# Performance work log

Hardware: AMD Instinct MI355X
Metric: run time of the kernel (lower is better)

## Reference

```python
import jax, jax.numpy as jnp
import numpy as np

H = 256
NUM_CONVS = 4
NUM_GRAPHS = 1024
N_PER_GRAPH = 32
ORDER = 3
NUM_TYPES = 22  # len(utils.BOND_TYPES)
NUM_NOISE_LEVEL = 50
ANNEAL_POWER = 2.0


def _build_graph():
    # Chain molecules extended to order-3 neighbors (mimics extend_graph on a path graph):
    # for |i-j| in [1,ORDER]: edge_order=|i-j|, edge_type = bond type if order 1 else NUM_TYPES+order-1.
    n = N_PER_GRAPH
    i, j = np.meshgrid(np.arange(n), np.arange(n), indexing='ij')
    dist = np.abs(i - j)
    mask = (dist >= 1) & (dist <= ORDER)
    src_l, dst_l, eo = i[mask], j[mask], dist[mask]
    offs = np.arange(NUM_GRAPHS)[:, None] * n
    src = (src_l[None, :] + offs).reshape(-1)
    dst = (dst_l[None, :] + offs).reshape(-1)
    edge_order = np.tile(eo, NUM_GRAPHS)
    rng = np.random.default_rng(0)
    bond_t = rng.integers(1, 5, size=edge_order.shape)
    edge_type = np.where(edge_order == 1, bond_t, NUM_TYPES + edge_order - 1)
    node2graph = np.repeat(np.arange(NUM_GRAPHS), n)
    return src, dst, edge_type, node2graph


def setup_inputs() -> dict:
    key = jax.random.key(0)
    ks = jax.random.split(key, 24)
    src, dst, edge_type, node2graph = _build_graph()
    N, E = node2graph.shape[0], src.shape[0]
    w = lambda k, s: (jax.random.normal(k, s, jnp.float32) * 0.05)
    sigmas = jnp.asarray(np.exp(np.linspace(np.log(10.0), np.log(0.01), NUM_NOISE_LEVEL)), dtype=jnp.float32)
    return {
        'atom_type': jnp.asarray(np.random.default_rng(1).integers(0, 100, N), jnp.int32),
        'edge_index': jnp.asarray(np.stack([src, dst]), jnp.int32),
        'edge_type': jnp.asarray(edge_type, jnp.int32),
        'node2graph': jnp.asarray(node2graph, jnp.int32),
        'noise_level': jax.random.randint(ks[0], (NUM_GRAPHS,), 0, NUM_NOISE_LEVEL, jnp.int32),
        'pos': jax.random.normal(ks[1], (N, 3), jnp.float32) * 3.0,
        'd_noise': jax.random.normal(ks[2], (E, 1), jnp.float32),
        'sigmas': sigmas,
        'node_emb': w(ks[3], (100, H)), 'edge_emb': w(ks[4], (100, H)),
        'in_W1': w(ks[5], (1, H)), 'in_b1': w(ks[6], (H,)),
        'in_W2': w(ks[7], (H, H)), 'in_b2': w(ks[8], (H,)),
        'gin_W1': w(ks[9], (NUM_CONVS, H, H)), 'gin_b1': w(ks[10], (NUM_CONVS, H)),
        'gin_W2': w(ks[11], (NUM_CONVS, H, H)), 'gin_b2': w(ks[12], (NUM_CONVS, H)),
        'out_W1': w(ks[13], (2 * H, H)), 'out_b1': w(ks[14], (H,)),
        'out_W2': w(ks[15], (H, H // 2)), 'out_b2': w(ks[16], (H // 2,)),
        'out_W3': w(ks[17], (H // 2, 1)), 'out_b3': w(ks[18], (1,)),
    }


def reference(atom_type, edge_index, edge_type, node2graph, noise_level,
              pos, d_noise, sigmas, node_emb, edge_emb,
              in_W1, in_b1, in_W2, in_b2,
              gin_W1, gin_b1, gin_W2, gin_b2,
              out_W1, out_b1, out_W2, out_b2, out_W3, out_b3):
    N = pos.shape[0]
    G = noise_level.shape[0]
    row, col = edge_index[0], edge_index[1]
    edge2graph = node2graph[row]                                  # [E]
    d = jnp.linalg.norm(pos[row] - pos[col], axis=-1, keepdims=True)  # [E,1]
    used_sigmas = sigmas[noise_level][edge2graph][:, None]        # [E,1]
    perturbed_d = d + d_noise * used_sigmas
    target = -(perturbed_d - d) / used_sigmas ** 2
    # embeddings + input MLP (Linear-relu-Linear)
    node_attr = node_emb[atom_type]                               # [N,H]
    d_emb = jax.nn.relu(perturbed_d @ in_W1 + in_b1) @ in_W2 + in_b2
    edge_attr = d_emb * edge_emb[edge_type]                       # [E,H]
    # GIN with GINE convs: agg = sum_j relu(x_j + e_ij); out = MLP(x + agg); relu between convs; residual
    x = node_attr
    n_convs = gin_W1.shape[0]
    for k in range(n_convs):
        msg = jax.nn.relu(x[row] + edge_attr)                     # [E,H]
        agg = jax.ops.segment_sum(msg, col, num_segments=N)       # [N,H]
        h = jax.nn.relu((x + agg) @ gin_W1[k] + gin_b1[k]) @ gin_W2[k] + gin_b2[k]
        if k < n_convs - 1:
            h = jax.nn.relu(h)
        x = h + x  # short_cut
    # edge score head
    feat = jnp.concatenate([x[row] * x[col], edge_attr], axis=-1)  # [E,2H]
    s = jax.nn.relu(feat @ out_W1 + out_b1)
    s = jax.nn.relu(s @ out_W2 + out_b2)
    s = s @ out_W3 + out_b3                                       # [E,1]
    scores = (s / used_sigmas).reshape(-1)
    t = target.reshape(-1)
    loss_e = 0.5 * (scores - t) ** 2 * used_sigmas.reshape(-1) ** ANNEAL_POWER
    return jax.ops.segment_sum(loss_e, edge2graph, num_segments=G)  # [G]
```

## Files before the change

### kernel.cpp

```cpp
#include <hip/hip_runtime.h>
#include <math.h>

typedef unsigned int u32;
typedef __attribute__((ext_vector_type(8))) short bf16x8;
typedef __attribute__((ext_vector_type(4))) float f32x4;

#define MFMA16(a,b,c) __builtin_amdgcn_mfma_f32_16x16x32_bf16(a,b,c,0,0,0)

__device__ inline u32 bf16r(float x){
  u32 u = __float_as_uint(x);
  return (u + 0x7fffu + ((u >> 16) & 1u)) >> 16;
}
__device__ inline u32 pack2(float a, float b){ return bf16r(a) | (bf16r(b) << 16); }
__device__ inline uint4 pack8(const float* f){
  uint4 v; v.x = pack2(f[0],f[1]); v.y = pack2(f[2],f[3]);
  v.z = pack2(f[4],f[5]); v.w = pack2(f[6],f[7]); return v;
}

__device__ __forceinline__ void gload_lds16(const void* g, void* l){
  __builtin_amdgcn_global_load_lds((const __attribute__((address_space(1))) unsigned int*)g,
                                   (__attribute__((address_space(3))) unsigned int*)l,
                                   16, 0, 0);
}

__device__ __forceinline__ int frag_off(int f, int quad){
  return (f>>1)*64 + (f&1)*32 + ((quad ^ ((f>>1)&3))*8);
}

__global__ void k_cvtAll(const float* __restrict__ inW2, const float* __restrict__ gW1,
                         const float* __restrict__ gW2, const float* __restrict__ oW1,
                         const float* __restrict__ oW2,
                         short* __restrict__ w2t, short* __restrict__ gw1t,
                         short* __restrict__ gw2t, short* __restrict__ ow1t,
                         short* __restrict__ ow2t){
  int gidx = blockIdx.x*256 + threadIdx.x;
  const float* src; short* dst; int t, K8, Nf;
  if (gidx < 8192)      { src = inW2; dst = w2t; t = gidx; K8 = 32; Nf = 256; }
  else if (gidx < 40960){ int r = gidx-8192;  int c = r>>13; t = r&8191;
                          src = gW1 + (size_t)c*65536; dst = gw1t + (size_t)c*65536; K8 = 32; Nf = 256; }
  else if (gidx < 73728){ int r = gidx-40960; int c = r>>13; t = r&8191;
                          src = gW2 + (size_t)c*65536; dst = gw2t + (size_t)c*65536; K8 = 32; Nf = 256; }
  else if (gidx < 90112){ t = gidx-73728; src = oW1; dst = ow1t; K8 = 64; Nf = 256; }
  else if (gidx < 94208){ t = gidx-90112; src = oW2; dst = ow2t; K8 = 32; Nf = 128; }
  else return;
  int f = t / K8, c = t - f*K8;
  float v[8];
  #pragma unroll
  for (int j=0;j<8;j++) v[j] = src[(size_t)(c*8+j)*Nf + f];
  ((uint4*)dst)[t] = pack8(v);
}

__global__ void k_pre(const int* __restrict__ ei, const int* __restrict__ n2g,
                      const int* __restrict__ nl, const float* __restrict__ sigmas,
                      const float* __restrict__ pos, const float* __restrict__ dn, int E,
                      float* __restrict__ pd, int* __restrict__ cnt, int* __restrict__ inlist){
  int e = blockIdx.x*256 + threadIdx.x;
  if (e >= E) return;
  int r = ei[e], c = ei[E+e];
  float sg = sigmas[nl[n2g[r]]];
  float dx = pos[3*r]-pos[3*c], dy = pos[3*r+1]-pos[3*c+1], dz = pos[3*r+2]-pos[3*c+2];
  float d = sqrtf(dx*dx + dy*dy + dz*dz);
  pd[e] = d + dn[e]*sg;
  int slot = atomicAdd(&cnt[c], 1);
  if (slot < 8) inlist[c*8 + slot] = e;
}

__global__ void k_ninit(const int* __restrict__ at, const float* __restrict__ nemb,
                        float* __restrict__ x, int N){
  int idx = blockIdx.x*256 + threadIdx.x;
  int i = idx >> 6, c = idx & 63;
  if (i >= N) return;
  ((float4*)x)[(size_t)i*64 + c] = ((const float4*)nemb)[(size_t)at[i]*64 + c];
}

__global__ __launch_bounds__(256) void k_attr(
    const float* __restrict__ pd, const float* __restrict__ W1, const float* __restrict__ b1,
    const short* __restrict__ W2t, const float* __restrict__ b2,
    const int* __restrict__ etype, const float* __restrict__ eemb,
    short* __restrict__ attr, int E)
{
  int tid = threadIdx.x;
  int base = blockIdx.x*64;
  int wv = tid>>6, lane = tid&63, quad = lane>>4, l15 = lane&15;
  float pdv[4];
  #pragma unroll
  for (int nt=0;nt<4;nt++) pdv[nt] = pd[base + nt*16 + l15];
  f32x4 acc[4][4];
  #pragma unroll
  for (int mt=0;mt<4;mt++) for (int nt=0;nt<4;nt++) acc[mt][nt] = (f32x4)0.f;
  #pragma unroll
  for (int s=0; s<8; s++){
    int k0 = s*32 + quad*8;
    float4 w1a = *(const float4*)(W1 + k0), w1b = *(const float4*)(W1 + k0 + 4);
    float4 b1a = *(const float4*)(b1 + k0), b1b = *(const float4*)(b1 + k0 + 4);
    bf16x8 a[4], b[4];
    #pragma unroll
    for (int mt=0;mt<4;mt++){
      int f = (wv*4+mt)*16 + l15;
      a[mt] = *(const bf16x8*)(W2t + (size_t)f*256 + k0);
    }
    #pragma unroll
    for (int nt=0;nt<4;nt++){
      float p = pdv[nt];
      float f[8] = {fmaxf(p*w1a.x+b1a.x,0.f), fmaxf(p*w1a.y+b1a.y,0.f),
                    fmaxf(p*w1a.z+b1a.z,0.f), fmaxf(p*w1a.w+b1a.w,0.f),
                    fmaxf(p*w1b.x+b1b.x,0.f), fmaxf(p*w1b.y+b1b.y,0.f),
                    fmaxf(p*w1b.z+b1b.z,0.f), fmaxf(p*w1b.w+b1b.w,0.f)};
      uint4 u = pack8(f);
      b[nt] = *(bf16x8*)&u;
    }
    #pragma unroll
    for (int mt=0;mt<4;mt++)
      #pragma unroll
      for (int nt=0;nt<4;nt++)
        acc[mt][nt] = MFMA16(a[mt], b[nt], acc[mt][nt]);
  }
  #pragma unroll
  for (int nt=0;nt<4;nt++){
    int e = base + nt*16 + l15;
    int et = etype[e];
    #pragma unroll
    for (int mt=0;mt<4;mt++){
      int f0 = (wv*4+mt)*16 + quad*4;
      float4 bb = *(const float4*)(b2 + f0);
      float4 em = *(const float4*)(eemb + (size_t)et*256 + f0);
      float v0 = (acc[mt][nt][0]+bb.x)*em.x, v1 = (acc[mt][nt][1]+bb.y)*em.y;
      float v2 = (acc[mt][nt][2]+bb.z)*em.z, v3 = (acc[mt][nt][3]+bb.w)*em.w;
      uint2 v; v.x = pack2(v0,v1); v.y = pack2(v2,v3);
      *(uint2*)(attr + (size_t)e*256 + f0) = v;
    }
  }
}

__global__ __launch_bounds__(256,3) void k_mlp(
    const float* __restrict__ x_in, const short* __restrict__ attrS,
    const int* __restrict__ ei, const int* __restrict__ cnt, const int* __restrict__ inlist,
    const short* __restrict__ W1t, const float* __restrict__ b1,
    const short* __restrict__ W2t, const float* __restrict__ b2,
    float* __restrict__ x_out, int N, int do_relu)
{
  __shared__ uint4 AlsV[64*32];
  short* Als = (short*)AlsV;
  short* T1  = Als;
  int tid = threadIdx.x;
  int base = blockIdx.x*64;
  for (int h=0; h<2; h++){
    int el = h*32 + (tid>>3), ch = tid&7;
    int j = base + el;
    float f[32];
    const float4* xj = (const float4*)x_in + (size_t)j*64 + ch*8;
    #pragma unroll
    for (int i=0;i<8;i++){ float4 v = xj[i]; f[i*4]=v.x; f[i*4+1]=v.y; f[i*4+2]=v.z; f[i*4+3]=v.w; }
    int deg = min(cnt[j], 8);
    for (int sIt=0; sIt<deg; sIt++){
      int e = inlist[j*8 + sIt];
      int r = ei[e];
      const float4* xr = (const float4*)x_in + (size_t)r*64 + ch*8;
      const short* ar = attrS + (size_t)e*256 + ch*32;
      #pragma unroll
      for (int i=0;i<8;i++){
        float4 xv = xr[i]; uint2 a = *(const uint2*)(ar + i*4);
        f[i*4]   += fmaxf(xv.x + __uint_as_float(a.x<<16), 0.f);
        f[i*4+1] += fmaxf(xv.y + __uint_as_float(a.x&0xffff0000u), 0.f);
        f[i*4+2] += fmaxf(xv.z + __uint_as_float(a.y<<16), 0.f);
        f[i*4+3] += fmaxf(xv.w + __uint_as_float(a.y&0xffff0000u), 0.f);
      }
    }
    #pragma unroll
    for (int qq=0;qq<4;qq++)
      *(uint4*)(Als + el*256 + (((ch*4+qq) ^ (el&7))*8)) = pack8(f + qq*8);
  }
  __syncthreads();
  int wv = tid>>6, lane = tid&63, quad = lane>>4, l15 = lane&15;
  f32x4 acc[4][4];
  #pragma unroll
  for (int mt=0;mt<4;mt++) for (int nt=0;nt<4;nt++) acc[mt][nt] = (f32x4)0.f;
  #pragma unroll
  for (int s=0; s<8; s++){
    bf16x8 a[4], b[4];
    #pragma unroll
    for (int mt=0;mt<4;mt++)
      a[mt] = *(const bf16x8*)(W1t + (size_t)((wv*4+mt)*16 + l15)*256 + s*32 + quad*8);
    #pragma unroll
    for (int nt=0;nt<4;nt++){
      int n = nt*16 + l15; int cc = s*4 + quad;
      b[nt] = *(const bf16x8*)(Als + n*256 + ((cc ^ (n&7))*8));
    }
    #pragma unroll
    for (int mt=0;mt<4;mt++)
      #pragma unroll
      for (int nt=0;nt<4;nt++)
        acc[mt][nt] = MFMA16(a[mt], b[nt], acc[mt][nt]);
  }
  __syncthreads();
  #pragma unroll
  for (int mt=0;mt<4;mt++){
    int f0 = (wv*4+mt)*16 + quad*4;
    float4 bb = *(const float4*)(b1 + f0);
    int c = f0 >> 3, off = (quad&1)*4;
    #pragma unroll
    for (int nt=0;nt<4;nt++){
      int n = nt*16 + l15;
      float v0 = fmaxf(acc[mt][nt][0]+bb.x,0.f), v1 = fmaxf(acc[mt][nt][1]+bb.y,0.f);
      float v2 = fmaxf(acc[mt][nt][2]+bb.z,0.f), v3 = fmaxf(acc[mt][nt][3]+bb.w,0.f);
      uint2 v; v.x = pack2(v0,v1); v.y = pack2(v2,v3);
      *(uint2*)(T1 + n*256 + ((c ^ (n&7))*8) + off) = v;
    }
  }
  __syncthreads();
  f32x4 acc2[4][4];
  #pragma unroll
  for (int mt=0;mt<4;mt++) for (int nt=0;nt<4;nt++) acc2[mt][nt] = (f32x4)0.f;
  #pragma unroll
  for (int s=0; s<8; s++){
    bf16x8 a[4], b[4];
    #pragma unroll
    for (int mt=0;mt<4;mt++)
      a[mt] = *(const bf16x8*)(W2t + (size_t)((wv*4+mt)*16 + l15)*256 + s*32 + quad*8);
    #pragma unroll
    for (int nt=0;nt<4;nt++){
      int n = nt*16 + l15; int cc = s*4 + quad;
      b[nt] = *(const bf16x8*)(T1 + n*256 + ((cc ^ (n&7))*8));
    }
    #pragma unroll
    for (int mt=0;mt<4;mt++)
      #pragma unroll
      for (int nt=0;nt<4;nt++)
        acc2[mt][nt] = MFMA16(a[mt], b[nt], acc2[mt][nt]);
  }
  #pragma unroll
  for (int mt=0;mt<4;mt++){
    int f0 = (wv*4+mt)*16 + quad*4;
    float4 bb = *(const float4*)(b2 + f0);
    #pragma unroll
    for (int nt=0;nt<4;nt++){
      int r = base + nt*16 + l15;
      const float* pin = x_in + (size_t)r*256 + f0;
      float* pout = x_out + (size_t)r*256 + f0;
      float4 xv = *(const float4*)pin;
      float h0 = acc2[mt][nt][0]+bb.x, h1 = acc2[mt][nt][1]+bb.y;
      float h2 = acc2[mt][nt][2]+bb.z, h3 = acc2[mt][nt][3]+bb.w;
      if (do_relu){ h0=fmaxf(h0,0.f); h1=fmaxf(h1,0.f); h2=fmaxf(h2,0.f); h3=fmaxf(h3,0.f); }
      xv.x += h0; xv.y += h1; xv.z += h2; xv.w += h3;
      *(float4*)pout = xv;
    }
  }
}

__global__ __launch_bounds__(256,2) void k_head(
    const float* __restrict__ x, const short* __restrict__ attrS,
    const int* __restrict__ ei,
    const short* __restrict__ W1t, const float* __restrict__ ob1,
    const short* __restrict__ W2t, const float* __restrict__ ob2,
    const float* __restrict__ W3, const float* __restrict__ ob3,
    const float* __restrict__ dnoise, const int* __restrict__ n2g,
    float* __restrict__ out, int E, int G)
{
  __shared__ uint4 BlsV[16*256];
  __shared__ float Sedge[64];
  __shared__ float part[4];
  short* Bls = (short*)BlsV;
  short* T   = (short*)BlsV;
  int tid = threadIdx.x;
  int base = blockIdx.x*64;
  int wv = tid>>6, lane = tid&63, quad = lane>>4, l15 = lane&15;
  if (tid < 64) Sedge[tid] = 0.f;
  if (tid < 4) part[tid] = 0.f;
  {
    int g = wv*64 + lane;
    int p = g>>3, hi = (g>>2)&1, cs = g&3;
    int n = p*2 + hi, cc = cs ^ (p&3);
    const short* srcb = attrS + (size_t)(base+n)*256 + cc*8;
    #pragma unroll
    for (int s=8; s<16; s++)
      gload_lds16(srcb + (s-8)*32, (char*)Bls + (size_t)s*4096 + wv*1024);
  }
  {
    int g = tid;
    int p = g>>3, hi = (g>>2)&1, cs = g&3;
    int n = p*2 + hi, cc = cs ^ (p&3);
    int rr = ei[base+n], rc = ei[E+base+n];
    const float* xr = x + (size_t)rr*256 + cc*8;
    const float* xc = x + (size_t)rc*256 + cc*8;
    #pragma unroll
    for (int s=0; s<8; s++){
      float4 a0 = *(const float4*)(xr + s*32), a1 = *(const float4*)(xr + s*32 + 4);
      float4 b0 = *(const float4*)(xc + s*32), b1 = *(const float4*)(xc + s*32 + 4);
      float f[8] = {a0.x*b0.x, a0.y*b0.y, a0.z*b0.z, a0.w*b0.w,
                    a1.x*b1.x, a1.y*b1.y, a1.z*b1.z, a1.w*b1.w};
      *(uint4*)(Bls + (size_t)s*2048 + g*8) = pack8(f);
    }
  }
  __syncthreads();
  f32x4 acc[4][4];
  #pragma unroll
  for (int mt=0;mt<4;mt++) for (int nt=0;nt<4;nt++) acc[mt][nt] = (f32x4)0.f;
  #pragma unroll
  for (int s=0; s<16; s++){
    bf16x8 a[4], b[4];
    #pragma unroll
    for (int mt=0;mt<4;mt++)
      a[mt] = *(const bf16x8*)(W1t + (size_t)((wv*4+mt)*16 + l15)*512 + s*32 + quad*8);
    #pragma unroll
    for (int nt=0;nt<4;nt++)
      b[nt] = *(const bf16x8*)(Bls + (size_t)s*2048 + frag_off(nt*16 + l15, quad));
    #pragma unroll
    for (int mt=0;mt<4;mt++)
      #pragma unroll
      for (int nt=0;nt<4;nt++)
        acc[mt][nt] = MFMA16(a[mt], b[nt], acc[mt][nt]);
  }
  __syncthreads();
  #pragma unroll
  for (int mt=0;mt<4;mt++){
    int f0 = (wv*4+mt)*16 + quad*4;
    float4 bb = *(const float4*)(ob1 + f0);
    int c = f0 >> 3, off = (quad&1)*4;
    #pragma unroll
    for (int nt=0;nt<4;nt++){
      int n = nt*16 + l15;
      float v0 = fmaxf(acc[mt][nt][0]+bb.x,0.f), v1 = fmaxf(acc[mt][nt][1]+bb.y,0.f);
      float v2 = fmaxf(acc[mt][nt][2]+bb.z,0.f), v3 = fmaxf(acc[mt][nt][3]+bb.w,0.f);
      uint2 v; v.x = pack2(v0,v1); v.y = pack2(v2,v3);
      *(uint2*)(T + n*256 + ((c ^ (n&7))*8) + off) = v;
    }
  }
  __syncthreads();
  f32x4 acc2[2][4];
  #pragma unroll
  for (int mt=0;mt<2;mt++) for (int nt=0;nt<4;nt++) acc2[mt][nt] = (f32x4)0.f;
  #pragma unroll
  for (int s=0; s<8; s++){
    bf16x8 a[2], b[4];
    #pragma unroll
    for (int mt=0;mt<2;mt++)
      a[mt] = *(const bf16x8*)(W2t + (size_t)((wv*2+mt)*16 + l15)*256 + s*32 + quad*8);
    #pragma unroll
    for (int nt=0;nt<4;nt++){
      int n = nt*16 + l15; int cc = s*4 + quad;
      b[nt] = *(const bf16x8*)(T + n*256 + ((cc ^ (n&7))*8));
    }
    #pragma unroll
    for (int mt=0;mt<2;mt++)
      #pragma unroll
      for (int nt=0;nt<4;nt++)
        acc2[mt][nt] = MFMA16(a[mt], b[nt], acc2[mt][nt]);
  }
  float4 b2v[2], w3v[2];
  #pragma unroll
  for (int mt=0;mt<2;mt++){
    int f0 = (wv*2+mt)*16 + quad*4;
    b2v[mt] = *(const float4*)(ob2 + f0);
    w3v[mt] = *(const float4*)(W3 + f0);
  }
  #pragma unroll
  for (int nt=0;nt<4;nt++){
    float p = 0.f;
    #pragma unroll
    for (int mt=0;mt<2;mt++){
      p += fmaxf(acc2[mt][nt][0]+b2v[mt].x,0.f)*w3v[mt].x;
      p += fmaxf(acc2[mt][nt][1]+b2v[mt].y,0.f)*w3v[mt].y;
      p += fmaxf(acc2[mt][nt][2]+b2v[mt].z,0.f)*w3v[mt].z;
      p += fmaxf(acc2[mt][nt][3]+b2v[mt].w,0.f)*w3v[mt].w;
    }
    p += __shfl_xor(p, 16);
    p += __shfl_xor(p, 32);
    if (lane < 16) atomicAdd(&Sedge[nt*16 + l15], p);
  }
  __syncthreads();
  int gbase = n2g[ei[base]];
  if (tid < 64){
    int e = base + tid;
    float sv = Sedge[tid] + ob3[0] + dnoise[e];
    float l = 0.5f*sv*sv;
    int g = n2g[ei[e]] - gbase;
    atomicAdd(&part[g & 3], l);
  }
  __syncthreads();
  if (tid < 2 && (gbase + tid) < G)
    atomicAdd(&out[gbase + tid], part[tid]);
}

static inline size_t alignup(size_t v){ return (v + 255) & ~(size_t)255; }

extern "C" void kernel_launch(void* const* d_in, const int* in_sizes, int n_in,
                              void* d_out, int out_size, void* d_ws, size_t ws_size,
                              hipStream_t stream) {
  const int*   at    = (const int*)  d_in[0];
  const int*   ei    = (const int*)  d_in[1];
  const int*   etype = (const int*)  d_in[2];
  const int*   n2g   = (const int*)  d_in[3];
  const int*   nl    = (const int*)  d_in[4];
  const float* pos   = (const float*)d_in[5];
  const float* dnoi  = (const float*)d_in[6];
  const float* sig   = (const float*)d_in[7];
  const float* nemb  = (const float*)d_in[8];
  const float* eemb  = (const float*)d_in[9];
  const float* inW1  = (const float*)d_in[10];
  const float* inb1  = (const float*)d_in[11];
  const float* inW2  = (const float*)d_in[12];
  const float* inb2  = (const float*)d_in[13];
  const float* gW1   = (const float*)d_in[14];
  const float* gb1   = (const float*)d_in[15];
  const float* gW2   = (const float*)d_in[16];
  const float* gb2   = (const float*)d_in[17];
  const float* oW1   = (const float*)d_in[18];
  const float* ob1   = (const float*)d_in[19];
  const float* oW2   = (const float*)d_in[20];
  const float* ob2   = (const float*)d_in[21];
  const float* oW3   = (const float*)d_in[22];
  const float* ob3   = (const float*)d_in[23];
  float* out = (float*)d_out;

  const int N = in_sizes[0];
  const int E = in_sizes[2];
  const int G = in_sizes[4];
  const int H = 256;

  char* w = (char*)d_ws;
  size_t off = 0;
  size_t o_attr  = off; off = alignup(off + (size_t)E*H*2);
  size_t o_xA    = off; off = alignup(off + (size_t)N*H*4);
  size_t o_xB    = off; off = alignup(off + (size_t)N*H*4);
  size_t o_pd    = off; off = alignup(off + (size_t)E*4);
  size_t o_cnt   = off; off = alignup(off + (size_t)N*4);
  size_t o_inl   = off; off = alignup(off + (size_t)N*8*4);
  size_t o_w2t   = off; off = alignup(off + (size_t)H*H*2);
  size_t o_gw1t  = off; off = alignup(off + (size_t)4*H*H*2);
  size_t o_gw2t  = off; off = alignup(off + (size_t)4*H*H*2);
  size_t o_ow1t  = off; off = alignup(off + (size_t)H*2*H*2);
  size_t o_ow2t  = off; off = alignup(off + (size_t)(H/2)*H*2);
  (void)ws_size; (void)n_in; (void)out_size;

  short* attrS = (short*)(w + o_attr);
  float* xA    = (float*)(w + o_xA);
  float* xB    = (float*)(w + o_xB);
  float* pd    = (float*)(w + o_pd);
  int*   cnt   = (int*)  (w + o_cnt);
  int*   inl   = (int*)  (w + o_inl);
  short* w2t   = (short*)(w + o_w2t);
  short* gw1t  = (short*)(w + o_gw1t);
  short* gw2t  = (short*)(w + o_gw2t);
  short* ow1t  = (short*)(w + o_ow1t);
  short* ow2t  = (short*)(w + o_ow2t);

  hipMemsetAsync(cnt, 0, (size_t)N*4, stream);
  hipMemsetAsync(out, 0, (size_t)G*4, stream);

  k_cvtAll<<<368, 256, 0, stream>>>(inW2, gW1, gW2, oW1, oW2,
                                    w2t, gw1t, gw2t, ow1t, ow2t);

  k_pre<<<(E+255)/256, 256, 0, stream>>>(ei, n2g, nl, sig, pos, dnoi, E, pd, cnt, inl);
  k_ninit<<<(N*64+255)/256, 256, 0, stream>>>(at, nemb, xA, N);
  k_attr<<<E/64, 256, 0, stream>>>(pd, inW1, inb1, w2t, inb2, etype, eemb, attrS, E);

  float* bufs[2] = {xA, xB};
  for (int c=0; c<4; c++){
    float* xin  = bufs[c & 1];
    float* xout = bufs[(c & 1) ^ 1];
    k_mlp<<<N/64, 256, 0, stream>>>(xin, attrS, ei, cnt, inl,
        gw1t + (size_t)c*H*H, gb1 + (size_t)c*H,
        gw2t + (size_t)c*H*H, gb2 + (size_t)c*H,
        xout, N, (c<3) ? 1 : 0);
  }

  k_head<<<E/64, 256, 0, stream>>>(xA, attrS, ei, ow1t, ob1, ow2t, ob2,
                                   oW3, ob3, dnoi, n2g, out, E, G);
}
```

Measured before the change: 583.6 us.

## Fuse node init and all four GIN convs into one per-graph kernel

Replaces the node-embedding init kernel and four per-conv MLP launches with a single kernel where each block owns one 32-node graph. Node features stay in LDS across all convs, so the global round trips of x between convs go away. The final features are written once as bf16, and the head reads that bf16 buffer. This relies on edges never crossing graphs (row index minus block base stays in 0..31), which holds because the inputs are separate graphs. Costs are smaller MFMA tiles (32 nodes per block instead of 64), extra LDS use that may limit occupancy, and bf16 rounding of the final x.

```diff
diff --git a/kernel.cpp b/kernel.cpp
--- a/kernel.cpp
+++ b/kernel.cpp
@@ -16,6 +16,7 @@
   uint4 v; v.x = pack2(f[0],f[1]); v.y = pack2(f[2],f[3]);
   v.z = pack2(f[4],f[5]); v.w = pack2(f[6],f[7]); return v;
 }
+__device__ inline float bf2f(short s){ return __uint_as_float(((u32)(unsigned short)s) << 16); }
 
 __device__ __forceinline__ void gload_lds16(const void* g, void* l){
   __builtin_amdgcn_global_load_lds((const __attribute__((address_space(1))) unsigned int*)g,
@@ -65,14 +66,6 @@
   if (slot < 8) inlist[c*8 + slot] = e;
 }
 
-__global__ void k_ninit(const int* __restrict__ at, const float* __restrict__ nemb,
-                        float* __restrict__ x, int N){
-  int idx = blockIdx.x*256 + threadIdx.x;
-  int i = idx >> 6, c = idx & 63;
-  if (i >= N) return;
-  ((float4*)x)[(size_t)i*64 + c] = ((const float4*)nemb)[(size_t)at[i]*64 + c];
-}
-
 __global__ __launch_bounds__(256) void k_attr(
     const float* __restrict__ pd, const float* __restrict__ W1, const float* __restrict__ b1,
     const short* __restrict__ W2t, const float* __restrict__ b2,
@@ -132,123 +125,163 @@
   }
 }
 
-__global__ __launch_bounds__(256,3) void k_mlp(
-    const float* __restrict__ x_in, const short* __restrict__ attrS,
-    const int* __restrict__ ei, const int* __restrict__ cnt, const int* __restrict__ inlist,
-    const short* __restrict__ W1t, const float* __restrict__ b1,
-    const short* __restrict__ W2t, const float* __restrict__ b2,
-    float* __restrict__ x_out, int N, int do_relu)
+__global__ __launch_bounds__(256,3) void k_conv4(
+    const int* __restrict__ at, const float* __restrict__ nemb,
+    const short* __restrict__ attrS, const int* __restrict__ ei,
+    const int* __restrict__ cnt, const int* __restrict__ inlist,
+    const short* __restrict__ gw1t, const float* __restrict__ gb1,
+    const short* __restrict__ gw2t, const float* __restrict__ gb2,
+    short* __restrict__ xF)
 {
-  __shared__ uint4 AlsV[64*32];
+  __shared__ float xls[32*256];
+  __shared__ uint4 AlsV[32*32];
   short* Als = (short*)AlsV;
   short* T1  = Als;
   int tid = threadIdx.x;
-  int base = blockIdx.x*64;
-  for (int h=0; h<2; h++){
-    int el = h*32 + (tid>>3), ch = tid&7;
-    int j = base + el;
+  int nbase = blockIdx.x*32;
+  int wv = tid>>6, lane = tid&63, quad = lane>>4, l15 = lane&15;
+  int jl = tid>>3, ch = tid&7;
+  {
+    int a = at[nbase + jl];
+    const float4* src = (const float4*)nemb + (size_t)a*64 + ch*8;
+    float* xrow = xls + jl*256;
+    int sw = jl&7;
+    #pragma unroll
+    for (int q=0;q<8;q++){
+      int g = ch*8 + q;
+      *(float4*)(xrow + ((g ^ sw)<<2)) = src[q];
+    }
+  }
+  __syncthreads();
+  for (int c=0; c<4; c++){
+    const short* W1t = gw1t + (size_t)c*65536;
+    const short* W2t = gw2t + (size_t)c*65536;
+    const float* b1 = gb1 + c*256;
+    const float* b2 = gb2 + c*256;
+    {
+      int j = nbase + jl;
+      float f[32];
+      const float* xrow = xls + jl*256;
+      int swj = jl&7;
+      #pragma unroll
+      for (int q=0;q<8;q++){
+        float4 v = *(const float4*)(xrow + (((ch*8+q) ^ swj)<<2));
+        f[q*4]=v.x; f[q*4+1]=v.y; f[q*4+2]=v.z; f[q*4+3]=v.w;
+      }
+      int deg = min(cnt[j], 8);
+      for (int sIt=0; sIt<deg; sIt++){
+        int e = inlist[j*8 + sIt];
+        int rl = ei[e] - nbase;
+        const float* xr = xls + rl*256;
+        int swr = rl&7;
+        const short* ar = attrS + (size_t)e*256 + ch*32;
+        #pragma unroll
+        for (int q=0;q<8;q++){
+          float4 xv = *(const float4*)(xr + (((ch*8+q) ^ swr)<<2));
+          uint2 a2 = *(const uint2*)(ar + q*4);
+          f[q*4]   += fmaxf(xv.x + __uint_as_float(a2.x<<16), 0.f);
+          f[q*4+1] += fmaxf(xv.y + __uint_as_float(a2.x&0xffff0000u), 0.f);
+          f[q*4+2] += fmaxf(xv.z + __uint_as_float(a2.y<<16), 0.f);
+          f[q*4+3] += fmaxf(xv.w + __uint_as_float(a2.y&0xffff0000u), 0.f);
+        }
+      }
+      #pragma unroll
+      for (int qq=0;qq<4;qq++)
+        *(uint4*)(Als + jl*256 + (((ch*4+qq) ^ (jl&7))*8)) = pack8(f + qq*8);
+    }
+    __syncthreads();
+    f32x4 acc[4][2];
+    #pragma unroll
+    for (int mt=0;mt<4;mt++) for (int nt=0;nt<2;nt++) acc[mt][nt] = (f32x4)0.f;
+    #pragma unroll
+    for (int s=0; s<8; s++){
+      bf16x8 a[4], b[2];
+      #pragma unroll
+      for (int mt=0;mt<4;mt++)
+        a[mt] = *(const bf16x8*)(W1t + (size_t)((wv*4+mt)*16 + l15)*256 + s*32 + quad*8);
+      #pragma unroll
+      for (int nt=0;nt<2;nt++){
+        int n = nt*16 + l15; int cc = s*4 + quad;
+        b[nt] = *(const bf16x8*)(Als + n*256 + ((cc ^ (n&7))*8));
+      }
+      #pragma unroll
+      for (int mt=0;mt<4;mt++)
+        #pragma unroll
+        for (int nt=0;nt<2;nt++)
+          acc[mt][nt] = MFMA16(a[mt], b[nt], acc[mt][nt]);
+    }
+    __syncthreads();
+    #pragma unroll
+    for (int mt=0;mt<4;mt++){
+      int f0 = (wv*4+mt)*16 + quad*4;
+      float4 bb = *(const float4*)(b1 + f0);
+      int cg = f0 >> 3, off = (quad&1)*4;
+      #pragma unroll
+      for (int nt=0;nt<2;nt++){
+        int n = nt*16 + l15;
+        float v0 = fmaxf(acc[mt][nt][0]+bb.x,0.f), v1 = fmaxf(acc[mt][nt][1]+bb.y,0.f);
+        float v2 = fmaxf(acc[mt][nt][2]+bb.z,0.f), v3 = fmaxf(acc[mt][nt][3]+bb.w,0.f);
+        uint2 v; v.x = pack2(v0,v1); v.y = pack2(v2,v3);
+        *(uint2*)(T1 + n*256 + ((cg ^ (n&7))*8) + off) = v;
+      }
+    }
+    __syncthreads();
+    f32x4 acc2[4][2];
+    #pragma unroll
+    for (int mt=0;mt<4;mt++) for (int nt=0;nt<2;nt++) acc2[mt][nt] = (f32x4)0.f;
+    #pragma unroll
+    for (int s=0; s<8; s++){
+      bf16x8 a[4], b[2];
+      #pragma unroll
+      for (int mt=0;mt<4;mt++)
+        a[mt] = *(const bf16x8*)(W2t + (size_t)((wv*4+mt)*16 + l15)*256 + s*32 + quad*8);
+      #pragma unroll
+      for (int nt=0;nt<2;nt++){
+        int n = nt*16 + l15; int cc = s*4 + quad;
+        b[nt] = *(const bf16x8*)(T1 + n*256 + ((cc ^ (n&7))*8));
+      }
+      #pragma unroll
+      for (int mt=0;mt<4;mt++)
+        #pragma unroll
+        for (int nt=0;nt<2;nt++)
+          acc2[mt][nt] = MFMA16(a[mt], b[nt], acc2[mt][nt]);
+    }
+    #pragma unroll
+    for (int mt=0;mt<4;mt++){
+      int f0 = (wv*4+mt)*16 + quad*4;
+      float4 bb = *(const float4*)(b2 + f0);
+      int g = f0 >> 2;
+      #pragma unroll
+      for (int nt=0;nt<2;nt++){
+        int n = nt*16 + l15;
+        float* px = xls + n*256 + ((g ^ (n&7))<<2);
+        float4 xv = *(float4*)px;
+        float h0 = acc2[mt][nt][0]+bb.x, h1 = acc2[mt][nt][1]+bb.y;
+        float h2 = acc2[mt][nt][2]+bb.z, h3 = acc2[mt][nt][3]+bb.w;
+        if (c < 3){ h0=fmaxf(h0,0.f); h1=fmaxf(h1,0.f); h2=fmaxf(h2,0.f); h3=fmaxf(h3,0.f); }
+        xv.x += h0; xv.y += h1; xv.z += h2; xv.w += h3;
+        *(float4*)px = xv;
+      }
+    }
+    __syncthreads();
+  }
+  {
+    const float* xrow = xls + jl*256;
+    int swj = jl&7;
     float f[32];
-    const float4* xj = (const float4*)x_in + (size_t)j*64 + ch*8;
-    #pragma unroll
-    for (int i=0;i<8;i++){ float4 v = xj[i]; f[i*4]=v.x; f[i*4+1]=v.y; f[i*4+2]=v.z; f[i*4+3]=v.w; }
-    int deg = min(cnt[j], 8);
-    for (int sIt=0; sIt<deg; sIt++){
-      int e = inlist[j*8 + sIt];
-      int r = ei[e];
-      const float4* xr = (const float4*)x_in + (size_t)r*64 + ch*8;
-      const short* ar = attrS + (size_t)e*256 + ch*32;
-      #pragma unroll
-      for (int i=0;i<8;i++){
-        float4 xv = xr[i]; uint2 a = *(const uint2*)(ar + i*4);
-        f[i*4]   += fmaxf(xv.x + __uint_as_float(a.x<<16), 0.f);
-        f[i*4+1] += fmaxf(xv.y + __uint_as_float(a.x&0xffff0000u), 0.f);
-        f[i*4+2] += fmaxf(xv.z + __uint_as_float(a.y<<16), 0.f);
-        f[i*4+3] += fmaxf(xv.w + __uint_as_float(a.y&0xffff0000u), 0.f);
-      }
+    #pragma unroll
+    for (int q=0;q<8;q++){
+      float4 v = *(const float4*)(xrow + (((ch*8+q) ^ swj)<<2));
+      f[q*4]=v.x; f[q*4+1]=v.y; f[q*4+2]=v.z; f[q*4+3]=v.w;
     }
     #pragma unroll
     for (int qq=0;qq<4;qq++)
-      *(uint4*)(Als + el*256 + (((ch*4+qq) ^ (el&7))*8)) = pack8(f + qq*8);
-  }
-  __syncthreads();
-  int wv = tid>>6, lane = tid&63, quad = lane>>4, l15 = lane&15;
-  f32x4 acc[4][4];
-  #pragma unroll
-  for (int mt=0;mt<4;mt++) for (int nt=0;nt<4;nt++) acc[mt][nt] = (f32x4)0.f;
-  #pragma unroll
-  for (int s=0; s<8; s++){
-    bf16x8 a[4], b[4];
-    #pragma unroll
-    for (int mt=0;mt<4;mt++)
-      a[mt] = *(const bf16x8*)(W1t + (size_t)((wv*4+mt)*16 + l15)*256 + s*32 + quad*8);
-    #pragma unroll
-    for (int nt=0;nt<4;nt++){
-      int n = nt*16 + l15; int cc = s*4 + quad;
-      b[nt] = *(const bf16x8*)(Als + n*256 + ((cc ^ (n&7))*8));
-    }
-    #pragma unroll
-    for (int mt=0;mt<4;mt++)
-      #pragma unroll
-      for (int nt=0;nt<4;nt++)
-        acc[mt][nt] = MFMA16(a[mt], b[nt], acc[mt][nt]);
-  }
-  __syncthreads();
-  #pragma unroll
-  for (int mt=0;mt<4;mt++){
-    int f0 = (wv*4+mt)*16 + quad*4;
-    float4 bb = *(const float4*)(b1 + f0);
-    int c = f0 >> 3, off = (quad&1)*4;
-    #pragma unroll
-    for (int nt=0;nt<4;nt++){
-      int n = nt*16 + l15;
-      float v0 = fmaxf(acc[mt][nt][0]+bb.x,0.f), v1 = fmaxf(acc[mt][nt][1]+bb.y,0.f);
-      float v2 = fmaxf(acc[mt][nt][2]+bb.z,0.f), v3 = fmaxf(acc[mt][nt][3]+bb.w,0.f);
-      uint2 v; v.x = pack2(v0,v1); v.y = pack2(v2,v3);
-      *(uint2*)(T1 + n*256 + ((c ^ (n&7))*8) + off) = v;
-    }
-  }
-  __syncthreads();
-  f32x4 acc2[4][4];
-  #pragma unroll
-  for (int mt=0;mt<4;mt++) for (int nt=0;nt<4;nt++) acc2[mt][nt] = (f32x4)0.f;
-  #pragma unroll
-  for (int s=0; s<8; s++){
-    bf16x8 a[4], b[4];
-    #pragma unroll
-    for (int mt=0;mt<4;mt++)
-      a[mt] = *(const bf16x8*)(W2t + (size_t)((wv*4+mt)*16 + l15)*256 + s*32 + quad*8);
-    #pragma unroll
-    for (int nt=0;nt<4;nt++){
-      int n = nt*16 + l15; int cc = s*4 + quad;
-      b[nt] = *(const bf16x8*)(T1 + n*256 + ((cc ^ (n&7))*8));
-    }
-    #pragma unroll
-    for (int mt=0;mt<4;mt++)
-      #pragma unroll
-      for (int nt=0;nt<4;nt++)
-        acc2[mt][nt] = MFMA16(a[mt], b[nt], acc2[mt][nt]);
-  }
-  #pragma unroll
-  for (int mt=0;mt<4;mt++){
-    int f0 = (wv*4+mt)*16 + quad*4;
-    float4 bb = *(const float4*)(b2 + f0);
-    #pragma unroll
-    for (int nt=0;nt<4;nt++){
-      int r = base + nt*16 + l15;
-      const float* pin = x_in + (size_t)r*256 + f0;
-      float* pout = x_out + (size_t)r*256 + f0;
-      float4 xv = *(const float4*)pin;
-      float h0 = acc2[mt][nt][0]+bb.x, h1 = acc2[mt][nt][1]+bb.y;
-      float h2 = acc2[mt][nt][2]+bb.z, h3 = acc2[mt][nt][3]+bb.w;
-      if (do_relu){ h0=fmaxf(h0,0.f); h1=fmaxf(h1,0.f); h2=fmaxf(h2,0.f); h3=fmaxf(h3,0.f); }
-      xv.x += h0; xv.y += h1; xv.z += h2; xv.w += h3;
-      *(float4*)pout = xv;
-    }
+      *(uint4*)(xF + (size_t)(nbase+jl)*256 + ch*32 + qq*8) = pack8(f + qq*8);
   }
 }
 
 __global__ __launch_bounds__(256,2) void k_head(
-    const float* __restrict__ x, const short* __restrict__ attrS,
+    const short* __restrict__ xF, const short* __restrict__ attrS,
     const int* __restrict__ ei,
     const short* __restrict__ W1t, const float* __restrict__ ob1,
     const short* __restrict__ W2t, const float* __restrict__ ob2,
@@ -280,14 +313,15 @@
     int p = g>>3, hi = (g>>2)&1, cs = g&3;
     int n = p*2 + hi, cc = cs ^ (p&3);
     int rr = ei[base+n], rc = ei[E+base+n];
-    const float* xr = x + (size_t)rr*256 + cc*8;
-    const float* xc = x + (size_t)rc*256 + cc*8;
+    const short* xr = xF + (size_t)rr*256 + cc*8;
+    const short* xc = xF + (size_t)rc*256 + cc*8;
     #pragma unroll
     for (int s=0; s<8; s++){
-      float4 a0 = *(const float4*)(xr + s*32), a1 = *(const float4*)(xr + s*32 + 4);
-      float4 b0 = *(const float4*)(xc + s*32), b1 = *(const float4*)(xc + s*32 + 4);
-      float f[8] = {a0.x*b0.x, a0.y*b0.y, a0.z*b0.z, a0.w*b0.w,
-                    a1.x*b1.x, a1.y*b1.y, a1.z*b1.z, a1.w*b1.w};
+      bf16x8 va = *(const bf16x8*)(xr + s*32);
+      bf16x8 vb = *(const bf16x8*)(xc + s*32);
+      float f[8];
+      #pragma unroll
+      for (int j=0;j<8;j++) f[j] = bf2f(va[j])*bf2f(vb[j]);
       *(uint4*)(Bls + (size_t)s*2048 + g*8) = pack8(f);
     }
   }
@@ -420,8 +454,7 @@
   char* w = (char*)d_ws;
   size_t off = 0;
   size_t o_attr  = off; off = alignup(off + (size_t)E*H*2);
-  size_t o_xA    = off; off = alignup(off + (size_t)N*H*4);
-  size_t o_xB    = off; off = alignup(off + (size_t)N*H*4);
+  size_t o_xF    = off; off = alignup(off + (size_t)N*H*2);
   size_t o_pd    = off; off = alignup(off + (size_t)E*4);
   size_t o_cnt   = off; off = alignup(off + (size_t)N*4);
   size_t o_inl   = off; off = alignup(off + (size_t)N*8*4);
@@ -433,8 +466,7 @@
   (void)ws_size; (void)n_in; (void)out_size;
 
   short* attrS = (short*)(w + o_attr);
-  float* xA    = (float*)(w + o_xA);
-  float* xB    = (float*)(w + o_xB);
+  short* xF    = (short*)(w + o_xF);
   float* pd    = (float*)(w + o_pd);
   int*   cnt   = (int*)  (w + o_cnt);
   int*   inl   = (int*)  (w + o_inl);
@@ -451,19 +483,11 @@
                                     w2t, gw1t, gw2t, ow1t, ow2t);
 
   k_pre<<<(E+255)/256, 256, 0, stream>>>(ei, n2g, nl, sig, pos, dnoi, E, pd, cnt, inl);
-  k_ninit<<<(N*64+255)/256, 256, 0, stream>>>(at, nemb, xA, N);
   k_attr<<<E/64, 256, 0, stream>>>(pd, inW1, inb1, w2t, inb2, etype, eemb, attrS, E);
 
-  float* bufs[2] = {xA, xB};
-  for (int c=0; c<4; c++){
-    float* xin  = bufs[c & 1];
-    float* xout = bufs[(c & 1) ^ 1];
-    k_mlp<<<N/64, 256, 0, stream>>>(xin, attrS, ei, cnt, inl,
-        gw1t + (size_t)c*H*H, gb1 + (size_t)c*H,
-        gw2t + (size_t)c*H*H, gb2 + (size_t)c*H,
-        xout, N, (c<3) ? 1 : 0);
-  }
-
-  k_head<<<E/64, 256, 0, stream>>>(xA, attrS, ei, ow1t, ob1, ow2t, ob2,
+  k_conv4<<<G, 256, 0, stream>>>(at, nemb, attrS, ei, cnt, inl,
+                                 gw1t, gb1, gw2t, gb2, xF);
+
+  k_head<<<E/64, 256, 0, stream>>>(xF, attrS, ei, ow1t, ob1, ow2t, ob2,
                                    oW3, ob3, dnoi, n2g, out, E, G);
 }
```

Measured after the change: 555.3 us. -4.9%, faster.
